# Kernel optimization log

Measured on AMD Instinct MI355X. Metric: run time of the kernel, lower is better.

## Reference

```python
import jax, jax.numpy as jnp
import numpy as np

Q = 200000       # number of logical qubits
C = 64           # number of cores
D = 128          # core_emb_shape == d_E == d_H


def setup_inputs() -> dict:
    key = jax.random.key(0)
    k1, k2, k3, k4, k5, k6 = jax.random.split(key, 6)
    prev_assign = jax.random.randint(k1, (Q,), 0, C)
    q_embeddings = jax.random.normal(k2, (Q, D), dtype=jnp.float32)
    padding_emb = jnp.zeros((D,), dtype=jnp.float32)
    # symmetric 0/1 core connectivity matrix
    a = (jax.random.uniform(k3, (C, C)) < 0.3).astype(jnp.float32)
    core_con = jnp.maximum(a, a.T) * (1.0 - jnp.eye(C, dtype=jnp.float32))
    # single GNN layer params: relu(X Wself + A X Wmsg + b)
    W_self = jax.random.normal(k4, (D, D), dtype=jnp.float32) / np.sqrt(D)
    W_msg = jax.random.normal(k5, (D, D), dtype=jnp.float32) / np.sqrt(D)
    b = jax.random.normal(k6, (D,), dtype=jnp.float32) * 0.01
    return {"prev_assign": prev_assign, "q_embeddings": q_embeddings,
            "padding_emb": padding_emb, "core_con": core_con,
            "W_self": W_self, "W_msg": W_msg, "b": b}


def reference(prev_assign, q_embeddings, padding_emb, core_con, W_self, W_msg, b):
    n_cores = core_con.shape[0]
    # fused per-core max-reduce over qubit embeddings grouped by prev_assign
    seg_max = jax.ops.segment_max(q_embeddings, prev_assign, num_segments=n_cores)  # [C, D]
    counts = jax.ops.segment_sum(jnp.ones((q_embeddings.shape[0],), q_embeddings.dtype),
                                 prev_assign, num_segments=n_cores)                 # [C]
    core_embs = jnp.where((counts > 0)[:, None], seg_max, padding_emb[None, :])     # [C, D]
    # GNN over core connectivity graph (single message-passing layer)
    msg = core_con @ (core_embs @ W_msg)            # [C, D]
    return jax.nn.relu(core_embs @ W_self + msg + b)  # [C, D]
```

## Files before the change

### kernel.cpp

```cpp
#include <hip/hip_runtime.h>
#include <math.h>

#define D 128
#define C 64
#define P1_THREADS 256
#define P1_GRID 512

__device__ __forceinline__ unsigned f2key(float f) {
  unsigned u = __float_as_uint(f);
  return (u & 0x80000000u) ? ~u : (u | 0x80000000u);
}
__device__ __forceinline__ float key2f(unsigned k) {
  unsigned u = (k & 0x80000000u) ? (k & 0x7fffffffu) : ~k;
  return __uint_as_float(u);
}

__global__ __launch_bounds__(P1_THREADS) void p1_segmax(
    const int* __restrict__ assign, const float* __restrict__ qe,
    unsigned* __restrict__ part, int Q, int niter) {
  __shared__ unsigned buf[C * D];
  int tid = threadIdx.x;
  for (int i = tid; i < C * D; i += P1_THREADS) buf[i] = 0u;
  __syncthreads();

  int lane = tid & 31;
  int r = tid >> 5;

  for (int it = blockIdx.x; it < niter; it += gridDim.x) {
    int base = it * 32;
    if (base + 32 <= Q) {
      float4 v[4];
      int a[4];
#pragma unroll
      for (int i = 0; i < 4; ++i) {
        int row = base + i * 8 + r;
        v[i] = *(const float4*)&qe[(size_t)row * D + lane * 4];
        a[i] = assign[row] * D + lane;
      }
#pragma unroll
      for (int i = 0; i < 4; ++i) {
        atomicMax(&buf[a[i] +  0], f2key(v[i].x));
        atomicMax(&buf[a[i] + 32], f2key(v[i].y));
        atomicMax(&buf[a[i] + 64], f2key(v[i].z));
        atomicMax(&buf[a[i] + 96], f2key(v[i].w));
      }
    } else {
      for (int i = 0; i < 4; ++i) {
        int row = base + i * 8 + r;
        if (row < Q) {
          float4 v = *(const float4*)&qe[(size_t)row * D + lane * 4];
          int a = assign[row] * D + lane;
          atomicMax(&buf[a +  0], f2key(v.x));
          atomicMax(&buf[a + 32], f2key(v.y));
          atomicMax(&buf[a + 64], f2key(v.z));
          atomicMax(&buf[a + 96], f2key(v.w));
        }
      }
    }
  }
  __syncthreads();

  unsigned* outp = part + (size_t)blockIdx.x * (C * D);
  for (int i = tid; i < C * D; i += P1_THREADS) {
    int d = i & 127;
    outp[i] = buf[(i & ~127) + (d & 3) * 32 + (d >> 2)];
  }
}

__global__ __launch_bounds__(256) void p2_merge(
    const unsigned* __restrict__ part, const float* __restrict__ padding,
    float* __restrict__ core_embs, int nb) {
  __shared__ unsigned red[256];
  int tid = threadIdx.x;
  int o_local = tid & 63;
  int rdr = tid >> 6;
  int o = blockIdx.x * 64 + o_local;
  unsigned m = 0u;
#pragma unroll 8
  for (int br = rdr; br < nb; br += 4)
    m = max(m, part[(size_t)br * (C * D) + o]);
  red[tid] = m;
  __syncthreads();
  if (tid < 64) {
    unsigned k = max(max(red[tid], red[tid + 64]),
                     max(red[tid + 128], red[tid + 192]));
    core_embs[o] = k ? key2f(k) : padding[o & (D - 1)];
  }
}

__global__ __launch_bounds__(D) void p3_fused(
    const float* __restrict__ core_embs, const float* __restrict__ con,
    const float* __restrict__ Wself, const float* __restrict__ Wmsg,
    const float* __restrict__ b, float* __restrict__ out) {
  __shared__ float CE[C * D];
  __shared__ float Mrow[D];
  __shared__ float crow[C];
  int t = threadIdx.x;
  int c = blockIdx.x;
  for (int i = t; i < C * D; i += D) CE[i] = core_embs[i];
  if (t < C) crow[t] = con[c * C + t];
  __syncthreads();
  float m = 0.f;
#pragma unroll 8
  for (int j = 0; j < C; ++j) m += crow[j] * CE[j * D + t];
  Mrow[t] = m;
  __syncthreads();
  float acc = b[t];
#pragma unroll 8
  for (int k = 0; k < D; ++k) acc += CE[c * D + k] * Wself[k * D + t];
#pragma unroll 8
  for (int k = 0; k < D; ++k) acc += Mrow[k] * Wmsg[k * D + t];
  out[c * D + t] = fmaxf(acc, 0.f);
}

extern "C" void kernel_launch(void* const* d_in, const int* in_sizes, int n_in,
                              void* d_out, int out_size, void* d_ws, size_t ws_size,
                              hipStream_t stream) {
  const int* assign    = (const int*)d_in[0];
  const float* qe      = (const float*)d_in[1];
  const float* padding = (const float*)d_in[2];
  const float* con     = (const float*)d_in[3];
  const float* Wself   = (const float*)d_in[4];
  const float* Wmsg    = (const float*)d_in[5];
  const float* b       = (const float*)d_in[6];
  float* out = (float*)d_out;
  int Q = in_sizes[0];

  const size_t slot = (size_t)C * D;
  size_t avail = ws_size / 4;
  long nb_max = (long)((avail > slot ? avail - slot : slot) / slot);
  int nb = (int)(nb_max < P1_GRID ? nb_max : P1_GRID);
  if (nb < 1) nb = 1;

  unsigned* part   = (unsigned*)d_ws;
  float* core_embs = (float*)((unsigned*)d_ws + (size_t)nb * slot);

  int niter = (Q + 31) / 32;

  hipLaunchKernelGGL(p1_segmax, dim3(nb), dim3(P1_THREADS), 0, stream,
                     assign, qe, part, Q, niter);
  hipLaunchKernelGGL(p2_merge, dim3((C * D) / 64), dim3(256), 0, stream,
                     part, padding, core_embs, nb);
  hipLaunchKernelGGL(p3_fused, dim3(C), dim3(D), 0, stream,
                     core_embs, con, Wself, Wmsg, b, out);
}
```

Before: 186.5 us.

## Fuse segmax, merge and GNN stages into one cooperative kernel with grid syncs

Replaces the three separate launches (per-block segment max, partial merge, GNN matmul) with a single cooperative kernel that uses grid-wide syncs between phases. The merge and GNN phases are redistributed across all resident blocks, and the GNN phase handles two cores per block. This removes two kernel launch gaps and inter-kernel drains. In exchange it requires all blocks to be co-resident, and it pays for grid-barrier synchronisation.

```diff
diff --git a/kernel.cpp b/kernel.cpp
--- a/kernel.cpp
+++ b/kernel.cpp
@@ -1,10 +1,13 @@
 #include <hip/hip_runtime.h>
+#include <hip/hip_cooperative_groups.h>
 #include <math.h>
+
+namespace cg = cooperative_groups;
 
 #define D 128
 #define C 64
-#define P1_THREADS 256
-#define P1_GRID 512
+#define NTHREADS 256
+#define MAXGRID 512
 
 __device__ __forceinline__ unsigned f2key(float f) {
   unsigned u = __float_as_uint(f);
@@ -15,12 +18,20 @@
   return __uint_as_float(u);
 }
 
-__global__ __launch_bounds__(P1_THREADS) void p1_segmax(
+__global__ __launch_bounds__(NTHREADS) void fused_all(
     const int* __restrict__ assign, const float* __restrict__ qe,
-    unsigned* __restrict__ part, int Q, int niter) {
+    unsigned* __restrict__ part, float* __restrict__ core_embs,
+    const float* __restrict__ padding, const float* __restrict__ con,
+    const float* __restrict__ Wself, const float* __restrict__ Wmsg,
+    const float* __restrict__ bias, float* __restrict__ out,
+    int Q, int niter, int nb) {
   __shared__ unsigned buf[C * D];
+  __shared__ unsigned red[NTHREADS];
+  __shared__ float MrowS[2][D];
+  __shared__ float crowS[2][C];
   int tid = threadIdx.x;
-  for (int i = tid; i < C * D; i += P1_THREADS) buf[i] = 0u;
+
+  for (int i = tid; i < C * D; i += NTHREADS) buf[i] = 0u;
   __syncthreads();
 
   int lane = tid & 31;
@@ -60,57 +71,56 @@
   }
   __syncthreads();
 
-  unsigned* outp = part + (size_t)blockIdx.x * (C * D);
-  for (int i = tid; i < C * D; i += P1_THREADS) {
-    int d = i & 127;
-    outp[i] = buf[(i & ~127) + (d & 3) * 32 + (d >> 2)];
+  {
+    unsigned* outp = part + (size_t)blockIdx.x * (C * D);
+    for (int i = tid; i < C * D; i += NTHREADS) {
+      int d = i & 127;
+      outp[i] = buf[(i & ~127) + (d & 3) * 32 + (d >> 2)];
+    }
   }
-}
 
-__global__ __launch_bounds__(256) void p2_merge(
-    const unsigned* __restrict__ part, const float* __restrict__ padding,
-    float* __restrict__ core_embs, int nb) {
-  __shared__ unsigned red[256];
-  int tid = threadIdx.x;
-  int o_local = tid & 63;
-  int rdr = tid >> 6;
-  int o = blockIdx.x * 64 + o_local;
-  unsigned m = 0u;
+  cg::this_grid().sync();
+
+  for (int ob = blockIdx.x * 32; ob < C * D; ob += gridDim.x * 32) {
+    int o = ob + (tid & 31);
+    int rdr = tid >> 5;
+    unsigned m = 0u;
 #pragma unroll 8
-  for (int br = rdr; br < nb; br += 4)
-    m = max(m, part[(size_t)br * (C * D) + o]);
-  red[tid] = m;
-  __syncthreads();
-  if (tid < 64) {
-    unsigned k = max(max(red[tid], red[tid + 64]),
-                     max(red[tid + 128], red[tid + 192]));
-    core_embs[o] = k ? key2f(k) : padding[o & (D - 1)];
+    for (int br = rdr; br < nb; br += 8)
+      m = max(m, part[(size_t)br * (C * D) + o]);
+    red[tid] = m;
+    __syncthreads();
+    if (tid < 32) {
+      unsigned k = m;
+#pragma unroll
+      for (int j = 1; j < 8; ++j) k = max(k, red[j * 32 + tid]);
+      core_embs[o] = k ? key2f(k) : padding[o & (D - 1)];
+    }
+    __syncthreads();
   }
-}
 
-__global__ __launch_bounds__(D) void p3_fused(
-    const float* __restrict__ core_embs, const float* __restrict__ con,
-    const float* __restrict__ Wself, const float* __restrict__ Wmsg,
-    const float* __restrict__ b, float* __restrict__ out) {
-  __shared__ float CE[C * D];
-  __shared__ float Mrow[D];
-  __shared__ float crow[C];
-  int t = threadIdx.x;
-  int c = blockIdx.x;
-  for (int i = t; i < C * D; i += D) CE[i] = core_embs[i];
-  if (t < C) crow[t] = con[c * C + t];
-  __syncthreads();
-  float m = 0.f;
+  cg::this_grid().sync();
+
+  float* CE = (float*)buf;
+  int half = tid >> 7;
+  int t = tid & 127;
+  for (int i = tid; i < C * D; i += NTHREADS) CE[i] = core_embs[i];
+
+  for (int c = blockIdx.x * 2 + half; c < C; c += gridDim.x * 2) {
+    if (t < C) crowS[half][t] = con[c * C + t];
+    __syncthreads();
+    float m = 0.f;
 #pragma unroll 8
-  for (int j = 0; j < C; ++j) m += crow[j] * CE[j * D + t];
-  Mrow[t] = m;
-  __syncthreads();
-  float acc = b[t];
+    for (int j = 0; j < C; ++j) m += crowS[half][j] * CE[j * D + t];
+    MrowS[half][t] = m;
+    __syncthreads();
+    float acc = bias[t];
 #pragma unroll 8
-  for (int k = 0; k < D; ++k) acc += CE[c * D + k] * Wself[k * D + t];
+    for (int k = 0; k < D; ++k) acc += CE[c * D + k] * Wself[k * D + t];
 #pragma unroll 8
-  for (int k = 0; k < D; ++k) acc += Mrow[k] * Wmsg[k * D + t];
-  out[c * D + t] = fmaxf(acc, 0.f);
+    for (int k = 0; k < D; ++k) acc += MrowS[half][k] * Wmsg[k * D + t];
+    out[c * D + t] = fmaxf(acc, 0.f);
+  }
 }
 
 extern "C" void kernel_launch(void* const* d_in, const int* in_sizes, int n_in,
@@ -122,14 +132,14 @@
   const float* con     = (const float*)d_in[3];
   const float* Wself   = (const float*)d_in[4];
   const float* Wmsg    = (const float*)d_in[5];
-  const float* b       = (const float*)d_in[6];
+  const float* bias    = (const float*)d_in[6];
   float* out = (float*)d_out;
   int Q = in_sizes[0];
 
   const size_t slot = (size_t)C * D;
   size_t avail = ws_size / 4;
   long nb_max = (long)((avail > slot ? avail - slot : slot) / slot);
-  int nb = (int)(nb_max < P1_GRID ? nb_max : P1_GRID);
+  int nb = (int)(nb_max < MAXGRID ? nb_max : MAXGRID);
   if (nb < 1) nb = 1;
 
   unsigned* part   = (unsigned*)d_ws;
@@ -137,10 +147,11 @@
 
   int niter = (Q + 31) / 32;
 
-  hipLaunchKernelGGL(p1_segmax, dim3(nb), dim3(P1_THREADS), 0, stream,
-                     assign, qe, part, Q, niter);
-  hipLaunchKernelGGL(p2_merge, dim3((C * D) / 64), dim3(256), 0, stream,
-                     part, padding, core_embs, nb);
-  hipLaunchKernelGGL(p3_fused, dim3(C), dim3(D), 0, stream,
-                     core_embs, con, Wself, Wmsg, b, out);
+  void* args[] = {
+    (void*)&assign, (void*)&qe, (void*)&part, (void*)&core_embs,
+    (void*)&padding, (void*)&con, (void*)&Wself, (void*)&Wmsg,
+    (void*)&bias, (void*)&out, (void*)&Q, (void*)&niter, (void*)&nb,
+  };
+  hipLaunchCooperativeKernel((void*)fused_all, dim3(nb), dim3(NTHREADS),
+                             args, 0, stream);
 }
```

Measured after the change: 317.7 us. 1.7x slower.
